# Kernel tuning notes

Measured on AMD Instinct MI355X. Metric: run time of the kernel, lower is better.

## Reference

```python
import jax, jax.numpy as jnp
import numpy as np
from jax import lax

B, N, M, NCLS = 16, 8192, 64, 80          # batch, anchors, GT boxes, classes
M_W, M_H = 640, 640                       # config.model_in_sz
CLASS_ID = 0                              # config.objective_class_id
PROB_T = 0.0                              # prob_threshold default
IOU_MATCH = 0.5                           # GT<->pred matching threshold
NMS_THR = 0.5                             # NMS IoU threshold
EPS = 1e-7


def xywh2xyxy(x):
    cx, cy, w, h = x[..., 0], x[..., 1], x[..., 2], x[..., 3]
    return jnp.stack([cx - w / 2, cy - h / 2, cx + w / 2, cy + h / 2], axis=-1)


def box_iou(a, b):
    # torchvision-style IoU (no +1), a: (M,4), b: (N,4) -> (M,N)
    area_a = (a[:, 2] - a[:, 0]) * (a[:, 3] - a[:, 1])
    area_b = (b[:, 2] - b[:, 0]) * (b[:, 3] - b[:, 1])
    lt = jnp.maximum(a[:, None, :2], b[None, :, :2])
    rb = jnp.minimum(a[:, None, 2:], b[None, :, 2:])
    wh = jnp.clip(rb - lt, 0)
    inter = wh[..., 0] * wh[..., 1]
    return inter / (area_a[:, None] + area_b[None, :] - inter)


def setup_inputs() -> dict:
    key = jax.random.key(0)
    k1, k2, k3, k4, k5 = jax.random.split(key, 5)
    # GT labels: [class_id, cx, cy, w, h] normalized to [0,1]
    cxy = jax.random.uniform(k1, (B, M, 2), minval=0.2, maxval=0.8)
    wh = jax.random.uniform(k2, (B, M, 2), minval=0.05, maxval=0.25)
    cls = jnp.zeros((B, M, 1), jnp.float32)
    label_batch = jnp.concatenate([cls, cxy, wh], axis=-1)  # (B, M, 5)
    # Predictions: each anchor is a GT box (pixel xywh) + small noise, so
    # IoU>=0.5 matching and NMS actually fire.
    gt_idx = jnp.arange(N) % M
    scale = jnp.array([M_W, M_H, M_W, M_H], jnp.float32)
    base = label_batch[:, gt_idx, 1:] * scale               # (B, N, 4)
    pred_xywh = base + jax.random.normal(k3, (B, N, 4)) * 2.0
    obj = jax.random.uniform(k4, (B, N, 1), minval=0.1, maxval=1.0)
    cls_logits = jax.random.uniform(k5, (B, N, NCLS))
    output = jnp.concatenate([pred_xywh, obj, cls_logits], axis=-1)  # (B,N,85)
    return {"output": output, "label_batch": label_batch}


def nms_keep(boxes, scores, valid):
    # Greedy NMS over a padded candidate set. `valid` marks real candidates;
    # invalid entries get -inf score and can never suppress anything.
    n = boxes.shape[0]
    order = jnp.argsort(jnp.where(valid, scores, -jnp.inf))[::-1]
    b = boxes[order]
    v = valid[order]
    x1, y1, x2, y2 = b[:, 0], b[:, 1], b[:, 2], b[:, 3]
    area = (x2 - x1 + 1) * (y2 - y1 + 1)   # +1 convention, as in the source nms
    pos = jnp.arange(n)

    def body(i, supp):
        active = v[i] & jnp.logical_not(supp[i])
        xx1 = jnp.maximum(x1[i], x1)
        yy1 = jnp.maximum(y1[i], y1)
        xx2 = jnp.minimum(x2[i], x2)
        yy2 = jnp.minimum(y2[i], y2)
        inter = jnp.clip(xx2 - xx1 + 1, 0) * jnp.clip(yy2 - yy1 + 1, 0)
        iou = inter / (area[i] + area - inter + EPS)
        return supp | (active & (pos > i) & (iou > NMS_THR))

    supp = lax.fori_loop(0, n, body, jnp.zeros(n, dtype=bool))
    return v & jnp.logical_not(supp), order


def _per_image(out, lab):
    pred_boxes = xywh2xyxy(out[:, :4])                      # (N,4) pixel xyxy
    obj = out[:, 4]
    logits = out[:, 5 + CLASS_ID] * obj                     # class prob * objectness
    scale = jnp.array([M_W, M_H, M_W, M_H], out.dtype)
    gt = jnp.clip(xywh2xyxy(lab[:, 1:]), 0, 1) * scale      # (M,4) pixel xyxy
    iou = box_iou(gt, pred_boxes)                           # (M,N)
    # candidate = passes prob threshold AND overlaps some GT with IoU>=0.5
    valid = (obj >= PROB_T) & jnp.any(iou >= IOU_MATCH, axis=0)
    keep, order = nms_keep(lax.stop_gradient(pred_boxes),
                           lax.stop_gradient(logits), valid)
    kept = keep.astype(out.dtype)
    return jnp.sum(logits[order] * kept) / jnp.sum(kept)


def reference(output, label_batch):
    loss = jax.vmap(_per_image)(output, label_batch)        # (B,)
    return loss[None, :]                                    # (1, B)
```

## Files before the change

### kernel.cpp

```cpp
#include <hip/hip_runtime.h>
#include <math.h>

#define BB 16
#define NN 8192
#define MM 64
#define ROW 85
#define EPS_F 1e-7f

#define NT1 256
#define NT2 1024
#define NW  16
#define CPW 4
#define CAPB 8

typedef unsigned long long u64;

__global__ void prep_kernel(const float* __restrict__ outp,
                            const float* __restrict__ lab,
                            float4* __restrict__ boxes,
                            float* __restrict__ keys) {
    __shared__ float4 gbox[MM];
    __shared__ float garea[MM];
    const int b = blockIdx.x;
    const int tid = threadIdx.x;
    if (tid < MM) {
        const float* lr = lab + ((size_t)b * MM + tid) * 5;
        float cx = lr[1], cy = lr[2], w = lr[3], h = lr[4];
        float x1 = fminf(fmaxf(cx - w * 0.5f, 0.f), 1.f) * 640.f;
        float y1 = fminf(fmaxf(cy - h * 0.5f, 0.f), 1.f) * 640.f;
        float x2 = fminf(fmaxf(cx + w * 0.5f, 0.f), 1.f) * 640.f;
        float y2 = fminf(fmaxf(cy + h * 0.5f, 0.f), 1.f) * 640.f;
        gbox[tid] = make_float4(x1, y1, x2, y2);
        garea[tid] = (x2 - x1) * (y2 - y1);
    }
    __syncthreads();
    const int n = blockIdx.y * NT1 + tid;
    const float* row = outp + ((size_t)b * NN + n) * ROW;
    float cx = row[0], cy = row[1], w = row[2], h = row[3];
    float obj = row[4], c0 = row[5];
    float px1 = cx - w * 0.5f, py1 = cy - h * 0.5f;
    float px2 = cx + w * 0.5f, py2 = cy + h * 0.5f;
    float pa = (px2 - px1) * (py2 - py1);

    const int m0 = n & (MM - 1);
    bool match;
    {
        float4 g = gbox[m0];
        float iw = fmaxf(fminf(px2, g.z) - fmaxf(px1, g.x), 0.f);
        float ih = fmaxf(fminf(py2, g.w) - fmaxf(py1, g.y), 0.f);
        float inter = iw * ih;
        match = (inter / (garea[m0] + pa - inter) >= 0.5f);
    }
    if (!match) {
        for (int m = 0; m < MM; ++m) {
            float4 g = gbox[m];
            float iw = fmaxf(fminf(px2, g.z) - fmaxf(px1, g.x), 0.f);
            float ih = fmaxf(fminf(py2, g.w) - fmaxf(py1, g.y), 0.f);
            float inter = iw * ih;
            match = match || (inter / (garea[m] + pa - inter) >= 0.5f);
        }
    }
    bool valid = (obj >= 0.0f) && match;
    size_t bn = (size_t)b * NN + ((n & 63) * 128 + (n >> 6));
    boxes[bn] = make_float4(px1, py1, px2, py2);
    keys[bn] = valid ? (c0 * obj) : -INFINITY;
}

__device__ __forceinline__ float wave_fold_max(float x) {
#define DPP_STEPX(ctrl)                                                          \
    { int _o = __builtin_amdgcn_update_dpp(__float_as_int(x), __float_as_int(x), \
                                           (ctrl), 0xF, 0xF, false);             \
      x = fmaxf(x, __int_as_float(_o)); }
    DPP_STEPX(0x111) DPP_STEPX(0x112) DPP_STEPX(0x114)
    DPP_STEPX(0x118) DPP_STEPX(0x142) DPP_STEPX(0x143)
#undef DPP_STEPX
    return x;
}
__device__ __forceinline__ float wave_fold_min(float x) {
#define DPP_STEPN(ctrl)                                                          \
    { int _o = __builtin_amdgcn_update_dpp(__float_as_int(x), __float_as_int(x), \
                                           (ctrl), 0xF, 0xF, false);             \
      x = fminf(x, __int_as_float(_o)); }
    DPP_STEPN(0x111) DPP_STEPN(0x112) DPP_STEPN(0x114)
    DPP_STEPN(0x118) DPP_STEPN(0x142) DPP_STEPN(0x143)
#undef DPP_STEPN
    return x;
}
__device__ __forceinline__ float wave_max64(float x) {
    return __int_as_float(__builtin_amdgcn_readlane(__float_as_int(wave_fold_max(x)), 63));
}
__device__ __forceinline__ float wave_sum64(float x) {
#define DPP_ADD(ctrl)                                                            \
    { int _o = __builtin_amdgcn_update_dpp(0, __float_as_int(x),                 \
                                           (ctrl), 0xF, 0xF, true);              \
      x += __int_as_float(_o); }
    DPP_ADD(0x111) DPP_ADD(0x112) DPP_ADD(0x114)
    DPP_ADD(0x118) DPP_ADD(0x142) DPP_ADD(0x143)
#undef DPP_ADD
    return __int_as_float(__builtin_amdgcn_readlane(__float_as_int(x), 63));
}
__device__ __forceinline__ float bcastlane(float v, int l) {
    return __int_as_float(__builtin_amdgcn_readlane(__float_as_int(v), l));
}

#define KILL_TEST(AK, K_)  do {                                                  \
    float _xx1 = fmaxf(bj.x, lx1[K_]), _yy1 = fmaxf(bj.y, ly1[K_]);              \
    float _xx2 = fminf(bj.z, lx2[K_]), _yy2 = fminf(bj.w, ly2[K_]);              \
    float _iw = fmaxf(_xx2 - _xx1 + 1.f, 0.f);                                   \
    float _ih = fmaxf(_yy2 - _yy1 + 1.f, 0.f);                                   \
    float _in = _iw * _ih;                                                       \
    if (sj > lps[K_] && 1.5f * _in > hbj + lha[K_]) (AK) = -INFINITY;            \
} while (0)

__global__ void __launch_bounds__(NT2)
nms_kernel(const float4* __restrict__ boxes, const float* __restrict__ keys,
           float* __restrict__ loss) {
    __shared__ float4 clusterBB[MM];
    __shared__ float  clusterMinA[MM];
    __shared__ float  topScore[MM];
    __shared__ int    slotCluster[MM];
    __shared__ u64    adjL[MM];
    __shared__ float4 keptBoxL[MM][CAPB];
    __shared__ float2 keptMetaL[MM][CAPB];
    __shared__ u64    kMask0[MM];
    __shared__ u64    kMask1[MM];
    __shared__ int    keptCnt[MM];
    __shared__ unsigned int chMask[3][2];
    __shared__ float  waveSum[NW];
    __shared__ int    waveCnt[NW];

    const int b = blockIdx.x;
    const int tid = threadIdx.x;
    const int wid = tid >> 6;
    const int lane = tid & 63;
    const size_t base = (size_t)b * NN;

#pragma unroll
    for (int q = 0; q < CPW; ++q) {
        const int c = CPW * wid + q;
        float mx = INFINITY, my = INFINITY, Mx = -INFINITY, My = -INFINITY;
        float mA = INFINITY, tS = -INFINITY;
#pragma unroll
        for (int s = 0; s < 2; ++s) {
            int idx = c * 128 + s * 64 + lane;
            float4 bb = boxes[base + idx];
            float sc = keys[base + idx];
            float ar = (bb.z - bb.x + 1.f) * (bb.w - bb.y + 1.f);
            if (sc != -INFINITY) {
                mx = fminf(mx, bb.x); my = fminf(my, bb.y);
                Mx = fmaxf(Mx, bb.z); My = fmaxf(My, bb.w);
                mA = fminf(mA, ar);   tS = fmaxf(tS, sc);
            }
        }
        mx = wave_fold_min(mx); my = wave_fold_min(my);
        Mx = wave_fold_max(Mx); My = wave_fold_max(My);
        mA = wave_fold_min(mA); tS = wave_fold_max(tS);
        if (lane == 63) {
            clusterBB[c] = make_float4(mx, my, Mx, My);
            clusterMinA[c] = mA;
            topScore[c] = tS;
        }
    }
    __syncthreads();

    if (wid == 0) {
        const int t = lane;
        float4 bbT = clusterBB[t];
        float  maT = clusterMinA[t];
        u64 adj = 0ull;
        for (int j = 0; j < MM; ++j) {
            float4 bbJ = clusterBB[j];
            float  maJ = clusterMinA[j];
            float iw = fminf(bbT.z, bbJ.z) - fmaxf(bbT.x, bbJ.x) + 1.f;
            float ih = fminf(bbT.w, bbJ.w) - fmaxf(bbT.y, bbJ.y) + 1.f;
            if (j != t && iw > 0.f && ih > 0.f) {
                float I = iw * ih;
                bool noe = (3.f * I < maT + maJ) || (2.f * I < fmaxf(maT, maJ));
                if (!noe) adj |= (1ull << j);
            }
        }
        adjL[t] = adj;
        kMask0[t] = 0ull; kMask1[t] = 0ull;
        keptCnt[t] = 0;
        float myS = topScore[t];
        int r = 0;
        for (int j = 0; j < MM; ++j) {
            float sj = topScore[j];
            r += (sj > myS || (sj == myS && j < t)) ? 1 : 0;
        }
        slotCluster[r] = t;
        if (t == 0) {
            chMask[0][0] = 0xFFFFFFFFu; chMask[0][1] = 0xFFFFFFFFu;
            chMask[1][0] = 0u; chMask[1][1] = 0u;
            chMask[2][0] = 0u; chMask[2][1] = 0u;
        }
    }
    __syncthreads();

    int cq[CPW];
#pragma unroll
    for (int q = 0; q < CPW; ++q) cq[q] = slotCluster[q * NW + wid];

    for (int rr = 0; rr < 8200; ++rr) {
        const int cur = rr % 3, nxt = (rr + 1) % 3, clr = (rr + 2) % 3;
        const u64 cm = ((u64)chMask[cur][1] << 32) | (u64)chMask[cur][0];
        if (cm == 0ull) break;
        if (tid == 0) { chMask[clr][0] = 0u; chMask[clr][1] = 0u; }
#pragma unroll
        for (int q = 0; q < CPW; ++q) {
            const int c = cq[q];
            if (((adjL[c] | (1ull << c)) & cm) == 0ull) continue;

            float lx1[2], ly1[2], lx2[2], ly2[2], lha[2], lps[2];
#pragma unroll
            for (int s = 0; s < 2; ++s) {
                int idx = c * 128 + s * 64 + lane;
                float4 bb = boxes[base + idx];
                lx1[s] = bb.x; ly1[s] = bb.y; lx2[s] = bb.z; ly2[s] = bb.w;
                lps[s] = keys[base + idx];
                lha[s] = 0.5f * ((lx2[s] - lx1[s] + 1.f) * (ly2[s] - ly1[s] + 1.f));
            }

            u64 om0 = kMask0[c], om1 = kMask1[c];
            float a0 = lps[0], a1 = lps[1];
            float4 CBc = clusterBB[c];
            float mha = 0.5f * clusterMinA[c];

            bool flag = false;
            {
                const u64 adjc = adjL[c];
                if ((adjc >> lane) & 1ull) {
                    int K = keptCnt[lane];
                    if (K > CAPB) flag = true;
                    int KB = K < CAPB ? K : CAPB;
#pragma unroll 4
                    for (int t2 = 0; t2 < KB; ++t2) {
                        float4 bj = keptBoxL[lane][t2];
                        float2 mt = keptMetaL[lane][t2];
                        float iwS = fminf(bj.z, CBc.z) - fmaxf(bj.x, CBc.x) + 1.f;
                        float ihS = fminf(bj.w, CBc.w) - fmaxf(bj.y, CBc.y) + 1.f;
                        if (iwS > 0.f && ihS > 0.f && 1.5f * (iwS * ihS) > mt.y + mha)
                            flag = true;
                    }
                }
            }
            u64 passM = __ballot(flag);

            while (passM) {
                int ac = __ffsll(passM) - 1; passM &= (passM - 1);
                int K = keptCnt[ac];
                int KB = K < CAPB ? K : CAPB;
#pragma unroll 4
                for (int t2 = 0; t2 < KB; ++t2) {
                    float4 bj = keptBoxL[ac][t2];
                    float2 mt = keptMetaL[ac][t2];
                    float iwS = fminf(bj.z, CBc.z) - fmaxf(bj.x, CBc.x) + 1.f;
                    float ihS = fminf(bj.w, CBc.w) - fmaxf(bj.y, CBc.y) + 1.f;
                    if (iwS > 0.f && ihS > 0.f && 1.5f * (iwS * ihS) > mt.y + mha) {
                        float sj = mt.x, hbj = mt.y;
                        KILL_TEST(a0, 0);
                        KILL_TEST(a1, 1);
                    }
                }
                if (K > CAPB) {
                    u64 mm = kMask0[ac];
                    while (mm) {
                        int bit = __ffsll(mm) - 1; mm &= (mm - 1);
                        int gi = ac * 128 + bit;
                        float4 bj = boxes[base + gi];
                        float sj = keys[base + gi];
                        float hbj = 0.5f * ((bj.z - bj.x + 1.f) * (bj.w - bj.y + 1.f))
                                    + 0.5f * EPS_F;
                        KILL_TEST(a0, 0);
                        KILL_TEST(a1, 1);
                    }
                    mm = kMask1[ac];
                    while (mm) {
                        int bit = __ffsll(mm) - 1; mm &= (mm - 1);
                        int gi = ac * 128 + 64 + bit;
                        float4 bj = boxes[base + gi];
                        float sj = keys[base + gi];
                        float hbj = 0.5f * ((bj.z - bj.x + 1.f) * (bj.w - bj.y + 1.f))
                                    + 0.5f * EPS_F;
                        KILL_TEST(a0, 0);
                        KILL_TEST(a1, 1);
                    }
                }
            }

            bool kept0 = false, kept1 = false;
            int cnt = 0;
            while (true) {
                float lv = fmaxf(a0, a1);
                float wm = wave_max64(lv);
                if (wm == -INFINITY) break;
                u64 bm = __ballot(lv == wm);
                int wl = __ffsll(bm) - 1;
                int la = (a0 == lv) ? 0 : 1;
                float cxa = la ? lx1[1] : lx1[0];
                float cya = la ? ly1[1] : ly1[0];
                float cxb = la ? lx2[1] : lx2[0];
                float cyb = la ? ly2[1] : ly2[0];
                float cha = la ? lha[1] : lha[0];
                float bx1 = bcastlane(cxa, wl), by1 = bcastlane(cya, wl);
                float bx2 = bcastlane(cxb, wl), by2 = bcastlane(cyb, wl);
                float hcb = bcastlane(cha, wl) + 0.5f * EPS_F;
                if (lane == wl) {
                    if (cnt < CAPB) {
                        keptBoxL[c][cnt] = make_float4(cxa, cya, cxb, cyb);
                        keptMetaL[c][cnt] = make_float2(lv, cha + 0.5f * EPS_F);
                    }
                    if (la == 0) { kept0 = true; a0 = -INFINITY; }
                    else         { kept1 = true; a1 = -INFINITY; }
                }
                cnt++;
                if (a0 != -INFINITY) {
                    float xx1 = fmaxf(bx1, lx1[0]), yy1 = fmaxf(by1, ly1[0]);
                    float xx2 = fminf(bx2, lx2[0]), yy2 = fminf(by2, ly2[0]);
                    float iw = fmaxf(xx2 - xx1 + 1.f, 0.f);
                    float ih = fmaxf(yy2 - yy1 + 1.f, 0.f);
                    if (1.5f * (iw * ih) > hcb + lha[0]) a0 = -INFINITY;
                }
                if (a1 != -INFINITY) {
                    float xx1 = fmaxf(bx1, lx1[1]), yy1 = fmaxf(by1, ly1[1]);
                    float xx2 = fminf(bx2, lx2[1]), yy2 = fminf(by2, ly2[1]);
                    float iw = fmaxf(xx2 - xx1 + 1.f, 0.f);
                    float ih = fmaxf(yy2 - yy1 + 1.f, 0.f);
                    if (1.5f * (iw * ih) > hcb + lha[1]) a1 = -INFINITY;
                }
            }
            u64 m0 = __ballot(kept0);
            u64 m1 = __ballot(kept1);
            if (lane == 0) {
                kMask0[c] = m0; kMask1[c] = m1; keptCnt[c] = cnt;
                if (m0 != om0 || m1 != om1)
                    atomicOr(&chMask[nxt][c >> 5], 1u << (c & 31));
            }
        }
        __syncthreads();
    }

    float s = 0.f; int ccount = 0;
#pragma unroll
    for (int q = 0; q < CPW; ++q) {
        const int c = cq[q];
        u64 m0 = kMask0[c], m1 = kMask1[c];
        if ((m0 >> lane) & 1ull) s += keys[base + c * 128 + lane];
        if ((m1 >> lane) & 1ull) s += keys[base + c * 128 + 64 + lane];
        ccount += (int)__popcll(m0) + (int)__popcll(m1);
    }
    s = wave_sum64(s);
    if (lane == 0) { waveSum[wid] = s; waveCnt[wid] = ccount; }
    __syncthreads();
    if (tid == 0) {
        float tot = 0.f; int ct = 0;
#pragma unroll
        for (int w = 0; w < NW; ++w) { tot += waveSum[w]; ct += waveCnt[w]; }
        loss[b] = tot / (float)ct;
    }
}

extern "C" void kernel_launch(void* const* d_in, const int* in_sizes, int n_in,
                              void* d_out, int out_size, void* d_ws, size_t ws_size,
                              hipStream_t stream) {
    const float* outp = (const float*)d_in[0];
    const float* lab  = (const float*)d_in[1];
    float* loss = (float*)d_out;

    float4* boxes = (float4*)d_ws;
    float*  keys  = (float*)((char*)d_ws + (size_t)BB * NN * sizeof(float4));

    dim3 g1(BB, NN / NT1);
    prep_kernel<<<g1, NT1, 0, stream>>>(outp, lab, boxes, keys);
    nms_kernel<<<BB, NT2, 0, stream>>>(boxes, keys, loss);
}
```

Measured before the change: 57.94 us.

## Add intra-round second pass over clusters whose neighbors changed, reordering loads

The per-cluster NMS body moves into a macro. Global box and key loads are issued before the adjacency pre-check so their latency can overlap it. After the first pass each round, a second pass reprocesses a wave's clusters whose adjacent clusters were already flagged as changed in the next-round mask. This aims to propagate suppression changes faster and cut the number of block-wide synchronized rounds. In exchange it adds redundant recomputation, reads chMask[nxt] while other waves are still writing it, and enlarges the code through macro duplication.

```diff
diff --git a/kernel.cpp b/kernel.cpp
--- a/kernel.cpp
+++ b/kernel.cpp
@@ -112,6 +112,137 @@
     if (sj > lps[K_] && 1.5f * _in > hbj + lha[K_]) (AK) = -INFINITY;            \
 } while (0)
 
+#define DO_CLUSTER(C_) do {                                                      \
+    const int c = (C_);                                                          \
+                       \
+    int _i0 = c * 128 + lane;                                                    \
+    float4 _bb0 = boxes[base + _i0];                                             \
+    float4 _bb1 = boxes[base + _i0 + 64];                                        \
+    float  _k0  = keys[base + _i0];                                              \
+    float  _k1  = keys[base + _i0 + 64];                                         \
+    u64 om0 = kMask0[c], om1 = kMask1[c];                                        \
+    float4 CBc = clusterBB[c];                                                   \
+    float mha = 0.5f * clusterMinA[c];                                           \
+                     \
+    bool _flag = false;                                                          \
+    {                                                                            \
+        const u64 _adjc = adjL[c];                                               \
+        if ((_adjc >> lane) & 1ull) {                                            \
+            int _K = keptCnt[lane];                                              \
+            if (_K > CAPB) _flag = true;                                         \
+            int _KB = _K < CAPB ? _K : CAPB;                                     \
+            _Pragma("unroll 4")                                                  \
+            for (int _t2 = 0; _t2 < _KB; ++_t2) {                                \
+                float4 _bj = keptBoxL[lane][_t2];                                \
+                float2 _mt = keptMetaL[lane][_t2];                               \
+                float _iwS = fminf(_bj.z, CBc.z) - fmaxf(_bj.x, CBc.x) + 1.f;    \
+                float _ihS = fminf(_bj.w, CBc.w) - fmaxf(_bj.y, CBc.y) + 1.f;    \
+                if (_iwS > 0.f && _ihS > 0.f && 1.5f * (_iwS * _ihS) > _mt.y + mha) \
+                    _flag = true;                                                \
+            }                                                                    \
+        }                                                                        \
+    }                                                                            \
+    u64 passM = __ballot(_flag);                                                 \
+                                                  \
+    float lx1[2] = { _bb0.x, _bb1.x }, ly1[2] = { _bb0.y, _bb1.y };              \
+    float lx2[2] = { _bb0.z, _bb1.z }, ly2[2] = { _bb0.w, _bb1.w };              \
+    float lps[2] = { _k0, _k1 };                                                 \
+    float lha[2] = { 0.5f * ((lx2[0] - lx1[0] + 1.f) * (ly2[0] - ly1[0] + 1.f)), \
+                     0.5f * ((lx2[1] - lx1[1] + 1.f) * (ly2[1] - ly1[1] + 1.f)) };\
+    float a0 = lps[0], a1 = lps[1];                                              \
+                                         \
+    while (passM) {                                                              \
+        int ac = __ffsll(passM) - 1; passM &= (passM - 1);                       \
+        int K = keptCnt[ac];                                                     \
+        int KB = K < CAPB ? K : CAPB;                                            \
+        _Pragma("unroll 4")                                                      \
+        for (int t2 = 0; t2 < KB; ++t2) {                                        \
+            float4 bj = keptBoxL[ac][t2];                                        \
+            float2 mt = keptMetaL[ac][t2];                                       \
+            float iwS = fminf(bj.z, CBc.z) - fmaxf(bj.x, CBc.x) + 1.f;           \
+            float ihS = fminf(bj.w, CBc.w) - fmaxf(bj.y, CBc.y) + 1.f;           \
+            if (iwS > 0.f && ihS > 0.f && 1.5f * (iwS * ihS) > mt.y + mha) {     \
+                float sj = mt.x, hbj = mt.y;                                     \
+                KILL_TEST(a0, 0);                                                \
+                KILL_TEST(a1, 1);                                                \
+            }                                                                    \
+        }                                                                        \
+        if (K > CAPB) {                               \
+            u64 mm = kMask0[ac];                                                 \
+            while (mm) {                                                         \
+                int bit = __ffsll(mm) - 1; mm &= (mm - 1);                       \
+                int gi = ac * 128 + bit;                                         \
+                float4 bj = boxes[base + gi];                                    \
+                float sj = keys[base + gi];                                      \
+                float hbj = 0.5f * ((bj.z - bj.x + 1.f) * (bj.w - bj.y + 1.f))   \
+                            + 0.5f * EPS_F;                                      \
+                KILL_TEST(a0, 0);                                                \
+                KILL_TEST(a1, 1);                                                \
+            }                                                                    \
+            mm = kMask1[ac];                                                     \
+            while (mm) {                                                         \
+                int bit = __ffsll(mm) - 1; mm &= (mm - 1);                       \
+                int gi = ac * 128 + 64 + bit;                                    \
+                float4 bj = boxes[base + gi];                                    \
+                float sj = keys[base + gi];                                      \
+                float hbj = 0.5f * ((bj.z - bj.x + 1.f) * (bj.w - bj.y + 1.f))   \
+                            + 0.5f * EPS_F;                                      \
+                KILL_TEST(a0, 0);                                                \
+                KILL_TEST(a1, 1);                                                \
+            }                                                                    \
+        }                                                                        \
+    }                                                                            \
+                              \
+    bool kept0 = false, kept1 = false;                                           \
+    int cnt = 0;                                                                 \
+    while (true) {                                                               \
+        float lv = fmaxf(a0, a1);                                                \
+        float wm = wave_max64(lv);                                               \
+        if (wm == -INFINITY) break;                                              \
+        u64 bm = __ballot(lv == wm);                                             \
+        int wl = __ffsll(bm) - 1;                                                \
+        int la = (a0 == lv) ? 0 : 1;                                             \
+        float cxa = la ? lx1[1] : lx1[0];                                        \
+        float cya = la ? ly1[1] : ly1[0];                                        \
+        float cxb = la ? lx2[1] : lx2[0];                                        \
+        float cyb = la ? ly2[1] : ly2[0];                                        \
+        float cha = la ? lha[1] : lha[0];                                        \
+        float bx1 = bcastlane(cxa, wl), by1 = bcastlane(cya, wl);                \
+        float bx2 = bcastlane(cxb, wl), by2 = bcastlane(cyb, wl);                \
+        float hcb = bcastlane(cha, wl) + 0.5f * EPS_F;                           \
+        if (lane == wl) {                                                        \
+            if (cnt < CAPB) {                                                    \
+                keptBoxL[c][cnt] = make_float4(cxa, cya, cxb, cyb);              \
+                keptMetaL[c][cnt] = make_float2(lv, cha + 0.5f * EPS_F);         \
+            }                                                                    \
+            if (la == 0) { kept0 = true; a0 = -INFINITY; }                       \
+            else         { kept1 = true; a1 = -INFINITY; }                       \
+        }                                                                        \
+        cnt++;                                                                   \
+        if (a0 != -INFINITY) {                                                   \
+            float xx1 = fmaxf(bx1, lx1[0]), yy1 = fmaxf(by1, ly1[0]);            \
+            float xx2 = fminf(bx2, lx2[0]), yy2 = fminf(by2, ly2[0]);            \
+            float iw = fmaxf(xx2 - xx1 + 1.f, 0.f);                              \
+            float ih = fmaxf(yy2 - yy1 + 1.f, 0.f);                              \
+            if (1.5f * (iw * ih) > hcb + lha[0]) a0 = -INFINITY;                 \
+        }                                                                        \
+        if (a1 != -INFINITY) {                                                   \
+            float xx1 = fmaxf(bx1, lx1[1]), yy1 = fmaxf(by1, ly1[1]);            \
+            float xx2 = fminf(bx2, lx2[1]), yy2 = fminf(by2, ly2[1]);            \
+            float iw = fmaxf(xx2 - xx1 + 1.f, 0.f);                              \
+            float ih = fmaxf(yy2 - yy1 + 1.f, 0.f);                              \
+            if (1.5f * (iw * ih) > hcb + lha[1]) a1 = -INFINITY;                 \
+        }                                                                        \
+    }                                                                            \
+    u64 m0 = __ballot(kept0);                                                    \
+    u64 m1 = __ballot(kept1);                                                    \
+    if (lane == 0) {                                                             \
+        kMask0[c] = m0; kMask1[c] = m1; keptCnt[c] = cnt;                        \
+        if (m0 != om0 || m1 != om1)                                              \
+            atomicOr(&chMask[nxt][c >> 5], 1u << (c & 31));                      \
+    }                                                                            \
+} while (0)
+
 __global__ void __launch_bounds__(NT2)
 nms_kernel(const float4* __restrict__ boxes, const float* __restrict__ keys,
            float* __restrict__ loss) {
@@ -208,134 +339,16 @@
         if (tid == 0) { chMask[clr][0] = 0u; chMask[clr][1] = 0u; }
 #pragma unroll
         for (int q = 0; q < CPW; ++q) {
-            const int c = cq[q];
-            if (((adjL[c] | (1ull << c)) & cm) == 0ull) continue;
-
-            float lx1[2], ly1[2], lx2[2], ly2[2], lha[2], lps[2];
-#pragma unroll
-            for (int s = 0; s < 2; ++s) {
-                int idx = c * 128 + s * 64 + lane;
-                float4 bb = boxes[base + idx];
-                lx1[s] = bb.x; ly1[s] = bb.y; lx2[s] = bb.z; ly2[s] = bb.w;
-                lps[s] = keys[base + idx];
-                lha[s] = 0.5f * ((lx2[s] - lx1[s] + 1.f) * (ly2[s] - ly1[s] + 1.f));
-            }
-
-            u64 om0 = kMask0[c], om1 = kMask1[c];
-            float a0 = lps[0], a1 = lps[1];
-            float4 CBc = clusterBB[c];
-            float mha = 0.5f * clusterMinA[c];
-
-            bool flag = false;
-            {
-                const u64 adjc = adjL[c];
-                if ((adjc >> lane) & 1ull) {
-                    int K = keptCnt[lane];
-                    if (K > CAPB) flag = true;
-                    int KB = K < CAPB ? K : CAPB;
-#pragma unroll 4
-                    for (int t2 = 0; t2 < KB; ++t2) {
-                        float4 bj = keptBoxL[lane][t2];
-                        float2 mt = keptMetaL[lane][t2];
-                        float iwS = fminf(bj.z, CBc.z) - fmaxf(bj.x, CBc.x) + 1.f;
-                        float ihS = fminf(bj.w, CBc.w) - fmaxf(bj.y, CBc.y) + 1.f;
-                        if (iwS > 0.f && ihS > 0.f && 1.5f * (iwS * ihS) > mt.y + mha)
-                            flag = true;
-                    }
-                }
-            }
-            u64 passM = __ballot(flag);
-
-            while (passM) {
-                int ac = __ffsll(passM) - 1; passM &= (passM - 1);
-                int K = keptCnt[ac];
-                int KB = K < CAPB ? K : CAPB;
-#pragma unroll 4
-                for (int t2 = 0; t2 < KB; ++t2) {
-                    float4 bj = keptBoxL[ac][t2];
-                    float2 mt = keptMetaL[ac][t2];
-                    float iwS = fminf(bj.z, CBc.z) - fmaxf(bj.x, CBc.x) + 1.f;
-                    float ihS = fminf(bj.w, CBc.w) - fmaxf(bj.y, CBc.y) + 1.f;
-                    if (iwS > 0.f && ihS > 0.f && 1.5f * (iwS * ihS) > mt.y + mha) {
-                        float sj = mt.x, hbj = mt.y;
-                        KILL_TEST(a0, 0);
-                        KILL_TEST(a1, 1);
-                    }
-                }
-                if (K > CAPB) {
-                    u64 mm = kMask0[ac];
-                    while (mm) {
-                        int bit = __ffsll(mm) - 1; mm &= (mm - 1);
-                        int gi = ac * 128 + bit;
-                        float4 bj = boxes[base + gi];
-                        float sj = keys[base + gi];
-                        float hbj = 0.5f * ((bj.z - bj.x + 1.f) * (bj.w - bj.y + 1.f))
-                                    + 0.5f * EPS_F;
-                        KILL_TEST(a0, 0);
-                        KILL_TEST(a1, 1);
-                    }
-                    mm = kMask1[ac];
-                    while (mm) {
-                        int bit = __ffsll(mm) - 1; mm &= (mm - 1);
-                        int gi = ac * 128 + 64 + bit;
-                        float4 bj = boxes[base + gi];
-                        float sj = keys[base + gi];
-                        float hbj = 0.5f * ((bj.z - bj.x + 1.f) * (bj.w - bj.y + 1.f))
-                                    + 0.5f * EPS_F;
-                        KILL_TEST(a0, 0);
-                        KILL_TEST(a1, 1);
-                    }
-                }
-            }
-
-            bool kept0 = false, kept1 = false;
-            int cnt = 0;
-            while (true) {
-                float lv = fmaxf(a0, a1);
-                float wm = wave_max64(lv);
-                if (wm == -INFINITY) break;
-                u64 bm = __ballot(lv == wm);
-                int wl = __ffsll(bm) - 1;
-                int la = (a0 == lv) ? 0 : 1;
-                float cxa = la ? lx1[1] : lx1[0];
-                float cya = la ? ly1[1] : ly1[0];
-                float cxb = la ? lx2[1] : lx2[0];
-                float cyb = la ? ly2[1] : ly2[0];
-                float cha = la ? lha[1] : lha[0];
-                float bx1 = bcastlane(cxa, wl), by1 = bcastlane(cya, wl);
-                float bx2 = bcastlane(cxb, wl), by2 = bcastlane(cyb, wl);
-                float hcb = bcastlane(cha, wl) + 0.5f * EPS_F;
-                if (lane == wl) {
-                    if (cnt < CAPB) {
-                        keptBoxL[c][cnt] = make_float4(cxa, cya, cxb, cyb);
-                        keptMetaL[c][cnt] = make_float2(lv, cha + 0.5f * EPS_F);
-                    }
-                    if (la == 0) { kept0 = true; a0 = -INFINITY; }
-                    else         { kept1 = true; a1 = -INFINITY; }
-                }
-                cnt++;
-                if (a0 != -INFINITY) {
-                    float xx1 = fmaxf(bx1, lx1[0]), yy1 = fmaxf(by1, ly1[0]);
-                    float xx2 = fminf(bx2, lx2[0]), yy2 = fminf(by2, ly2[0]);
-                    float iw = fmaxf(xx2 - xx1 + 1.f, 0.f);
-                    float ih = fmaxf(yy2 - yy1 + 1.f, 0.f);
-                    if (1.5f * (iw * ih) > hcb + lha[0]) a0 = -INFINITY;
-                }
-                if (a1 != -INFINITY) {
-                    float xx1 = fmaxf(bx1, lx1[1]), yy1 = fmaxf(by1, ly1[1]);
-                    float xx2 = fminf(bx2, lx2[1]), yy2 = fminf(by2, ly2[1]);
-                    float iw = fmaxf(xx2 - xx1 + 1.f, 0.f);
-                    float ih = fmaxf(yy2 - yy1 + 1.f, 0.f);
-                    if (1.5f * (iw * ih) > hcb + lha[1]) a1 = -INFINITY;
-                }
-            }
-            u64 m0 = __ballot(kept0);
-            u64 m1 = __ballot(kept1);
-            if (lane == 0) {
-                kMask0[c] = m0; kMask1[c] = m1; keptCnt[c] = cnt;
-                if (m0 != om0 || m1 != om1)
-                    atomicOr(&chMask[nxt][c >> 5], 1u << (c & 31));
-            }
+            const int c1 = cq[q];
+            if (((adjL[c1] | (1ull << c1)) & cm) == 0ull) continue;
+            DO_CLUSTER(c1);
+        }
+#pragma unroll
+        for (int q = 0; q < CPW; ++q) {
+            const int c2 = cq[q];
+            const u64 g2 = ((u64)chMask[nxt][1] << 32) | (u64)chMask[nxt][0];
+            if ((adjL[c2] & g2) == 0ull) continue;
+            DO_CLUSTER(c2);
         }
         __syncthreads();
     }
```

After: 62.35 us. 7.6% more time.
